# Performance work log

Measured on AMD Instinct MI355X. Metric: run time of the kernel, lower is better.

## Reference

```python
import jax, jax.numpy as jnp
import numpy as np

B, F_IN, T, N = 2, 32, 8, 20000
E = 320000
HID, F_OUT = 64, 32


def setup_inputs() -> dict:
    key = jax.random.key(0)
    ks = jax.random.split(key, 8)
    x = jax.random.normal(ks[0], (B, F_IN, T, N), dtype=jnp.float32)
    edge_index = jax.random.randint(ks[1], (2, E), 0, N, dtype=jnp.int64)
    edge_weight = jax.random.uniform(ks[2], (E,), dtype=jnp.float32)
    # GCNConv params (glorot weights, zero bias)
    s1 = float(np.sqrt(6.0 / (F_IN + HID)))
    s2 = float(np.sqrt(6.0 / (HID + F_OUT)))
    W1 = jax.random.uniform(ks[3], (F_IN, HID), minval=-s1, maxval=s1, dtype=jnp.float32)
    b1 = jnp.zeros((HID,), jnp.float32)
    W2 = jax.random.uniform(ks[4], (HID, F_OUT), minval=-s2, maxval=s2, dtype=jnp.float32)
    b2 = jnp.zeros((F_OUT,), jnp.float32)
    return {"x": x, "edge_index": edge_index, "edge_weight": edge_weight,
            "W1": W1, "b1": b1, "W2": W2, "b2": b2}


def reference(x, edge_index, edge_weight, W1, b1, W2, b2):
    Bb, Fin, Tt, Nn = x.shape
    row, col = edge_index[0], edge_index[1]
    # gcn_norm with self loops (fill value 1.0)
    loop = jnp.arange(Nn)
    row_f = jnp.concatenate([row, loop])
    col_f = jnp.concatenate([col, loop])
    ew_f = jnp.concatenate([edge_weight, jnp.ones((Nn,), x.dtype)])
    deg = jnp.zeros((Nn,), x.dtype).at[col_f].add(ew_f)
    deg_inv_sqrt = jnp.where(deg > 0, 1.0 / jnp.sqrt(jnp.where(deg > 0, deg, 1.0)), 0.0)
    norm = deg_inv_sqrt[row_f] * ew_f * deg_inv_sqrt[col_f]  # [E+N]

    # fold (batch, time) together: every time step uses the same graph
    h = x.transpose(0, 2, 3, 1).reshape(Bb * Tt, Nn, Fin)  # [BT, N, F]

    def gcn_conv(h, W, b):
        h = h @ W                                   # linear first (as in GCNConv)
        msg = h[:, row_f, :] * norm[None, :, None]  # gather + weight  [BT, E+N, C]
        agg = jnp.zeros_like(h).at[:, col_f, :].add(msg)  # scatter-add over targets
        return agg + b

    h = gcn_conv(h, W1, b1)      # dropout(p=0.1) is identity in eval mode
    h = jnp.tanh(gcn_conv(h, W2, b2))
    # back to [B, out_channels, T, N]
    return h.reshape(Bb, Tt, Nn, -1).transpose(0, 3, 1, 2)
```

## Files before the change

### kernel.cpp

```cpp
#include <hip/hip_runtime.h>
#include <hip/hip_bf16.h>
#include <hip/hip_fp16.h>

#define NB    2
#define FIN   32
#define TT    8
#define NN    20000
#define BT    16
#define CC    32
#define ROW   512
#define ELLK  64

typedef unsigned int nvec4 __attribute__((ext_vector_type(4)));

__global__ __launch_bounds__(256) void prep_kernel(const float* __restrict__ x,
                                                   __half* __restrict__ xt,
                                                   const int* __restrict__ ei,
                                                   const float* __restrict__ ew,
                                                   float* __restrict__ deg,
                                                   const float* __restrict__ W1,
                                                   const float* __restrict__ W2,
                                                   const float* __restrict__ b1,
                                                   float* __restrict__ W12T,
                                                   float* __restrict__ bb,
                                                   int N, int E, int gtr, int ge) {
    __shared__ float tile[128][33];
    int bid = blockIdx.x;
    if (bid < gtr) {
        int bt = bid & 15;
        int b = bt >> 3, t = bt & 7;
        int n0 = (bid >> 4) * 128;
        for (int i = 0; i < 16; ++i) {
            int idx = i * 256 + threadIdx.x;
            int f = idx >> 7;
            int nl = idx & 127;
            int n = n0 + nl;
            float v = (n < N) ? x[(size_t)(b * 256 + f * 8 + t) * N + n] : 0.f;
            tile[nl][f] = v;
        }
        __syncthreads();
        for (int i = 0; i < 8; ++i) {
            int idx = i * 256 + threadIdx.x;
            int nl = idx >> 4, f2 = idx & 15;
            int n = n0 + nl;
            if (n < N) {
                __half2 h = __floats2half2_rn(tile[nl][f2 * 2], tile[nl][f2 * 2 + 1]);
                *(__half2*)(xt + (size_t)n * ROW + bt * 32 + f2 * 2) = h;
            }
        }
    } else if (bid < gtr + ge) {
        int e = (bid - gtr) * 256 + threadIdx.x;
        if (e < E) {
            int c = ei[E + e];
            atomicAdd(&deg[c], ew[e]);
        }
    } else {
        for (int i = threadIdx.x; i < 1024; i += 256) {
            int f = i >> 5, c = i & 31;
            float acc = 0.f;
            for (int k = 0; k < 64; ++k) acc += W1[f * 64 + k] * W2[k * 32 + c];
            W12T[c * 32 + f] = acc;
            if (f == 0) {
                float a2 = 0.f;
                for (int k = 0; k < 64; ++k) a2 += b1[k] * W2[k * 32 + c];
                bb[c] = a2;
            }
        }
    }
}

__global__ void fill_kernel(const int* __restrict__ ei, const float* __restrict__ ew,
                            const float* __restrict__ deg,
                            int* __restrict__ fill, int2* __restrict__ ell, int E) {
    int e = blockIdx.x * 256 + threadIdx.x;
    if (e >= E) return;
    int r = ei[e], c = ei[E + e];
    float w = rsqrtf(deg[r] + 1.0f) * ew[e] * rsqrtf(deg[c] + 1.0f);
    int p = atomicAdd(&fill[c], 1);
    if (p < ELLK) ell[(size_t)c * ELLK + p] = make_int2(r, __float_as_int(w));
}

__device__ inline void unpack8n(const nvec4& u, float* f) {
    union { unsigned int v; __half2 h; } c;
    float2 a;
    c.v = u.x; a = __half22float2(c.h); f[0] = a.x; f[1] = a.y;
    c.v = u.y; a = __half22float2(c.h); f[2] = a.x; f[3] = a.y;
    c.v = u.z; a = __half22float2(c.h); f[4] = a.x; f[5] = a.y;
    c.v = u.w; a = __half22float2(c.h); f[6] = a.x; f[7] = a.y;
}

template <bool PASS1>
__global__ __launch_bounds__(256) void agg16_kernel(const __half* __restrict__ src,
                                                    __half* __restrict__ dst,
                                                    const float* __restrict__ deg,
                                                    const int* __restrict__ fillcnt,
                                                    const int2* __restrict__ ell,
                                                    float* __restrict__ rowsum,
                                                    int N) {
    int n = (blockIdx.x * 256 + threadIdx.x) >> 6;
    if (n >= N) return;
    int lane = threadIdx.x & 63;
    int cnt = fillcnt[n];
    if (cnt > ELLK) cnt = ELLK;
    float sw = 1.0f / (deg[n] + 1.0f);
    const int2* row = ell + (size_t)n * ELLK;
    float acc[8];
    {
        nvec4 u = *(const nvec4*)(src + (size_t)n * ROW + lane * 8);
        float f[8]; unpack8n(u, f);
#pragma unroll
        for (int j = 0; j < 8; ++j) acc[j] = sw * f[j];
    }
    float sumw = 0.f;
    int e = 0;
    for (; e + 8 <= cnt; e += 8) {
        long long raw[8];
#pragma unroll
        for (int j = 0; j < 8; ++j)
            raw[j] = __builtin_nontemporal_load((const long long*)(row + e + j));
        nvec4 u[8];
#pragma unroll
        for (int j = 0; j < 8; ++j) {
            unsigned int sn = (unsigned int)(raw[j] & 0xffffffffll);
            u[j] = *(const nvec4*)(src + (size_t)sn * ROW + lane * 8);
        }
#pragma unroll
        for (int j = 0; j < 8; ++j) {
            float f[8]; unpack8n(u[j], f);
            float w = __int_as_float((int)(raw[j] >> 32));
            if (PASS1) sumw += w;
#pragma unroll
            for (int q = 0; q < 8; ++q) acc[q] += w * f[q];
        }
    }
    for (; e + 2 <= cnt; e += 2) {
        long long rA = __builtin_nontemporal_load((const long long*)(row + e));
        long long rB = __builtin_nontemporal_load((const long long*)(row + e + 1));
        nvec4 uA = *(const nvec4*)(src + (size_t)(unsigned int)(rA & 0xffffffffll) * ROW + lane * 8);
        nvec4 uB = *(const nvec4*)(src + (size_t)(unsigned int)(rB & 0xffffffffll) * ROW + lane * 8);
        float fA[8], fB[8]; unpack8n(uA, fA); unpack8n(uB, fB);
        float wA = __int_as_float((int)(rA >> 32)), wB = __int_as_float((int)(rB >> 32));
        if (PASS1) sumw += wA + wB;
#pragma unroll
        for (int q = 0; q < 8; ++q) acc[q] += wA * fA[q];
#pragma unroll
        for (int q = 0; q < 8; ++q) acc[q] += wB * fB[q];
    }
    if (e < cnt) {
        long long r = __builtin_nontemporal_load((const long long*)(row + e));
        nvec4 u = *(const nvec4*)(src + (size_t)(unsigned int)(r & 0xffffffffll) * ROW + lane * 8);
        float f[8]; unpack8n(u, f);
        float w = __int_as_float((int)(r >> 32));
        if (PASS1) sumw += w;
#pragma unroll
        for (int q = 0; q < 8; ++q) acc[q] += w * f[q];
    }
    if (PASS1 && lane == 0) rowsum[n] = sw + sumw;
    union { nvec4 u; __half2 h[4]; } o;
    o.h[0] = __floats2half2_rn(acc[0], acc[1]);
    o.h[1] = __floats2half2_rn(acc[2], acc[3]);
    o.h[2] = __floats2half2_rn(acc[4], acc[5]);
    o.h[3] = __floats2half2_rn(acc[6], acc[7]);
    __builtin_nontemporal_store(o.u, (nvec4*)(dst + (size_t)n * ROW + lane * 8));
}

__global__ __launch_bounds__(256) void final_kernel(const __half* __restrict__ Z,
                                                    const float* __restrict__ W12T,
                                                    const float* __restrict__ bb,
                                                    const float* __restrict__ b2,
                                                    const float* __restrict__ rowsum,
                                                    float* __restrict__ out, int N) {
    __shared__ float zt[64][36];
    __shared__ float wT[32][36];
    __shared__ float bbs[32], b2s[32], rs[64];
    int bt = blockIdx.y;
    int b = bt >> 3, t = bt & 7;
    int n0 = blockIdx.x * 64;
    int tid = threadIdx.x;
    for (int i = tid; i < 1024; i += 256) wT[i >> 5][i & 31] = W12T[i];
    if (tid < 32) { bbs[tid] = bb[tid]; b2s[tid] = b2[tid]; }
    if (tid < 64) { int n = n0 + tid; rs[tid] = (n < N) ? rowsum[n] : 0.f; }
    for (int i = tid; i < 1024; i += 256) {
        int nl = i >> 4, f2 = i & 15;
        int n = n0 + nl;
        float2 v = make_float2(0.f, 0.f);
        if (n < N) {
            __half2 h = *(const __half2*)(Z + (size_t)n * ROW + bt * 32 + f2 * 2);
            v = __half22float2(h);
        }
        zt[nl][f2 * 2] = v.x;
        zt[nl][f2 * 2 + 1] = v.y;
    }
    __syncthreads();
    int c = tid & 31;
    int g = tid >> 5;
    float w[32];
#pragma unroll
    for (int k = 0; k < 8; ++k) {
        float4 v = *(const float4*)&wT[c][k * 4];
        w[k * 4 + 0] = v.x; w[k * 4 + 1] = v.y; w[k * 4 + 2] = v.z; w[k * 4 + 3] = v.w;
    }
    float cb2 = b2s[c], cbb = bbs[c];
    float res[8];
#pragma unroll
    for (int i = 0; i < 8; ++i) {
        int nl = g * 8 + i;
        float acc = cb2 + rs[nl] * cbb;
#pragma unroll
        for (int k = 0; k < 8; ++k) {
            float4 z4 = *(const float4*)&zt[nl][k * 4];
            acc = fmaf(z4.x, w[k * 4 + 0], acc);
            acc = fmaf(z4.y, w[k * 4 + 1], acc);
            acc = fmaf(z4.z, w[k * 4 + 2], acc);
            acc = fmaf(z4.w, w[k * 4 + 3], acc);
        }
        res[i] = tanhf(acc);
    }
    __syncthreads();
#pragma unroll
    for (int i = 0; i < 8; ++i) {
        int nl = g * 8 + i;
        zt[nl][(c + nl) & 31] = res[i];
    }
    __syncthreads();
    for (int i = tid; i < 2048; i += 256) {
        int cc = i >> 6, nl = i & 63;
        int n = n0 + nl;
        if (n < N) out[(((size_t)b * 32 + cc) * TT + t) * (size_t)NN + n] = zt[nl][(cc + nl) & 31];
    }
}

extern "C" void kernel_launch(void* const* d_in, const int* in_sizes, int n_in,
                              void* d_out, int out_size, void* d_ws, size_t ws_size,
                              hipStream_t stream) {
    const float* x  = (const float*)d_in[0];
    const int*   ei = (const int*)d_in[1];
    const float* ew = (const float*)d_in[2];
    const float* W1 = (const float*)d_in[3];
    const float* b1 = (const float*)d_in[4];
    const float* W2 = (const float*)d_in[5];
    const float* b2 = (const float*)d_in[6];
    float* out = (float*)d_out;

    const int N = NN;
    const int E = in_sizes[2];

    char* p = (char*)d_ws;
    __half* xt = (__half*)p;  p += (size_t)N * ROW * 2;
    __half* Y  = (__half*)p;  p += (size_t)N * ROW * 2;
    __half* Z  = (__half*)p;  p += (size_t)N * ROW * 2;
    int2*  ell     = (int2*)p;   p += (size_t)N * ELLK * 8;
    float* deg     = (float*)p;  p += (size_t)N * 4;
    int*   fill    = (int*)p;    p += (size_t)N * 4;
    float* rowsum  = (float*)p;  p += (size_t)N * 4;
    float* W12T    = (float*)p;  p += 1024 * 4;
    float* bb      = (float*)p;

    (void)hipMemsetAsync(deg, 0, (size_t)N * 4 * 2, stream);

    int ge  = (E + 255) / 256;
    int gtr = ((N + 127) / 128) * BT;
    prep_kernel<<<gtr + ge + 1, 256, 0, stream>>>(x, xt, ei, ew, deg,
                                                  W1, W2, b1, W12T, bb, N, E, gtr, ge);
    fill_kernel<<<ge, 256, 0, stream>>>(ei, ew, deg, fill, ell, E);

    int gagg = (N * 64 + 255) / 256;
    agg16_kernel<true ><<<gagg, 256, 0, stream>>>(xt, Y, deg, fill, ell, rowsum, N);
    agg16_kernel<false><<<gagg, 256, 0, stream>>>(Y, Z, deg, fill, ell, rowsum, N);

    dim3 gfin((N + 63) / 64, BT);
    final_kernel<<<gfin, 256, 0, stream>>>(Z, W12T, bb, b2, rowsum, out, N);
}
```

Baseline: 189.8 us.

## Fuse ELL fill into prep kernel and pack edges as 16-bit index plus fp16 weight

Removes the separate fill kernel by building the ELL adjacency inside prep_kernel, storing the raw edge weight instead of the normalized one, since degrees are not yet final at that point. Each ELL entry shrinks from 8 bytes to 4, packing a 16-bit source index with an fp16 weight. The aggregation kernels now recompute the normalization per edge from deg[src] and the destination degree. This cuts one launch and halves ELL traffic, at the cost of an extra gather of deg per edge, some rsqrt work, and fp16 weight precision. A 16-bit index cannot hold node ids above 65535; N=20000 fits, but the code would break for larger graphs.

```diff
diff --git a/kernel.cpp b/kernel.cpp
--- a/kernel.cpp
+++ b/kernel.cpp
@@ -13,11 +13,19 @@
 
 typedef unsigned int nvec4 __attribute__((ext_vector_type(4)));
 
+__device__ inline float h16tof(unsigned int hi) {
+    union { unsigned short u; __half h; } cv;
+    cv.u = (unsigned short)hi;
+    return __half2float(cv.h);
+}
+
 __global__ __launch_bounds__(256) void prep_kernel(const float* __restrict__ x,
                                                    __half* __restrict__ xt,
                                                    const int* __restrict__ ei,
                                                    const float* __restrict__ ew,
                                                    float* __restrict__ deg,
+                                                   int* __restrict__ fill,
+                                                   unsigned int* __restrict__ ell,
                                                    const float* __restrict__ W1,
                                                    const float* __restrict__ W2,
                                                    const float* __restrict__ b1,
@@ -51,8 +59,15 @@
     } else if (bid < gtr + ge) {
         int e = (bid - gtr) * 256 + threadIdx.x;
         if (e < E) {
-            int c = ei[E + e];
-            atomicAdd(&deg[c], ew[e]);
+            int r = ei[e], c = ei[E + e];
+            float wf = ew[e];
+            atomicAdd(&deg[c], wf);
+            int p = atomicAdd(&fill[c], 1);
+            if (p < ELLK) {
+                union { __half h; unsigned short u; } cv;
+                cv.h = __float2half_rn(wf);
+                ell[(size_t)c * ELLK + p] = ((unsigned int)cv.u << 16) | (unsigned int)r;
+            }
         }
     } else {
         for (int i = threadIdx.x; i < 1024; i += 256) {
@@ -69,17 +84,6 @@
     }
 }
 
-__global__ void fill_kernel(const int* __restrict__ ei, const float* __restrict__ ew,
-                            const float* __restrict__ deg,
-                            int* __restrict__ fill, int2* __restrict__ ell, int E) {
-    int e = blockIdx.x * 256 + threadIdx.x;
-    if (e >= E) return;
-    int r = ei[e], c = ei[E + e];
-    float w = rsqrtf(deg[r] + 1.0f) * ew[e] * rsqrtf(deg[c] + 1.0f);
-    int p = atomicAdd(&fill[c], 1);
-    if (p < ELLK) ell[(size_t)c * ELLK + p] = make_int2(r, __float_as_int(w));
-}
-
 __device__ inline void unpack8n(const nvec4& u, float* f) {
     union { unsigned int v; __half2 h; } c;
     float2 a;
@@ -94,7 +98,7 @@
                                                     __half* __restrict__ dst,
                                                     const float* __restrict__ deg,
                                                     const int* __restrict__ fillcnt,
-                                                    const int2* __restrict__ ell,
+                                                    const unsigned int* __restrict__ ell,
                                                     float* __restrict__ rowsum,
                                                     int N) {
     int n = (blockIdx.x * 256 + threadIdx.x) >> 6;
@@ -102,8 +106,10 @@
     int lane = threadIdx.x & 63;
     int cnt = fillcnt[n];
     if (cnt > ELLK) cnt = ELLK;
-    float sw = 1.0f / (deg[n] + 1.0f);
-    const int2* row = ell + (size_t)n * ELLK;
+    float dn = deg[n] + 1.0f;
+    float dc = rsqrtf(dn);
+    float sw = 1.0f / dn;
+    const unsigned int* row = ell + (size_t)n * ELLK;
     float acc[8];
     {
         nvec4 u = *(const nvec4*)(src + (size_t)n * ROW + lane * 8);
@@ -114,32 +120,37 @@
     float sumw = 0.f;
     int e = 0;
     for (; e + 8 <= cnt; e += 8) {
-        long long raw[8];
+        unsigned int raw[8];
 #pragma unroll
         for (int j = 0; j < 8; ++j)
-            raw[j] = __builtin_nontemporal_load((const long long*)(row + e + j));
+            raw[j] = __builtin_nontemporal_load(row + e + j);
         nvec4 u[8];
+        float dg[8];
 #pragma unroll
         for (int j = 0; j < 8; ++j) {
-            unsigned int sn = (unsigned int)(raw[j] & 0xffffffffll);
+            unsigned int sn = raw[j] & 0xffffu;
             u[j] = *(const nvec4*)(src + (size_t)sn * ROW + lane * 8);
+            dg[j] = deg[sn];
         }
 #pragma unroll
         for (int j = 0; j < 8; ++j) {
+            float w = rsqrtf(dg[j] + 1.0f) * h16tof(raw[j] >> 16) * dc;
+            if (PASS1) sumw += w;
             float f[8]; unpack8n(u[j], f);
-            float w = __int_as_float((int)(raw[j] >> 32));
-            if (PASS1) sumw += w;
 #pragma unroll
             for (int q = 0; q < 8; ++q) acc[q] += w * f[q];
         }
     }
     for (; e + 2 <= cnt; e += 2) {
-        long long rA = __builtin_nontemporal_load((const long long*)(row + e));
-        long long rB = __builtin_nontemporal_load((const long long*)(row + e + 1));
-        nvec4 uA = *(const nvec4*)(src + (size_t)(unsigned int)(rA & 0xffffffffll) * ROW + lane * 8);
-        nvec4 uB = *(const nvec4*)(src + (size_t)(unsigned int)(rB & 0xffffffffll) * ROW + lane * 8);
+        unsigned int rA = __builtin_nontemporal_load(row + e);
+        unsigned int rB = __builtin_nontemporal_load(row + e + 1);
+        unsigned int sA = rA & 0xffffu, sB = rB & 0xffffu;
+        nvec4 uA = *(const nvec4*)(src + (size_t)sA * ROW + lane * 8);
+        nvec4 uB = *(const nvec4*)(src + (size_t)sB * ROW + lane * 8);
+        float dgA = deg[sA], dgB = deg[sB];
         float fA[8], fB[8]; unpack8n(uA, fA); unpack8n(uB, fB);
-        float wA = __int_as_float((int)(rA >> 32)), wB = __int_as_float((int)(rB >> 32));
+        float wA = rsqrtf(dgA + 1.0f) * h16tof(rA >> 16) * dc;
+        float wB = rsqrtf(dgB + 1.0f) * h16tof(rB >> 16) * dc;
         if (PASS1) sumw += wA + wB;
 #pragma unroll
         for (int q = 0; q < 8; ++q) acc[q] += wA * fA[q];
@@ -147,10 +158,11 @@
         for (int q = 0; q < 8; ++q) acc[q] += wB * fB[q];
     }
     if (e < cnt) {
-        long long r = __builtin_nontemporal_load((const long long*)(row + e));
-        nvec4 u = *(const nvec4*)(src + (size_t)(unsigned int)(r & 0xffffffffll) * ROW + lane * 8);
+        unsigned int r = __builtin_nontemporal_load(row + e);
+        unsigned int sn = r & 0xffffu;
+        nvec4 u = *(const nvec4*)(src + (size_t)sn * ROW + lane * 8);
+        float w = rsqrtf(deg[sn] + 1.0f) * h16tof(r >> 16) * dc;
         float f[8]; unpack8n(u, f);
-        float w = __int_as_float((int)(r >> 32));
         if (PASS1) sumw += w;
 #pragma unroll
         for (int q = 0; q < 8; ++q) acc[q] += w * f[q];
@@ -249,7 +261,7 @@
     __half* xt = (__half*)p;  p += (size_t)N * ROW * 2;
     __half* Y  = (__half*)p;  p += (size_t)N * ROW * 2;
     __half* Z  = (__half*)p;  p += (size_t)N * ROW * 2;
-    int2*  ell     = (int2*)p;   p += (size_t)N * ELLK * 8;
+    unsigned int* ell = (unsigned int*)p; p += (size_t)N * ELLK * 4;
     float* deg     = (float*)p;  p += (size_t)N * 4;
     int*   fill    = (int*)p;    p += (size_t)N * 4;
     float* rowsum  = (float*)p;  p += (size_t)N * 4;
@@ -260,9 +272,8 @@
 
     int ge  = (E + 255) / 256;
     int gtr = ((N + 127) / 128) * BT;
-    prep_kernel<<<gtr + ge + 1, 256, 0, stream>>>(x, xt, ei, ew, deg,
+    prep_kernel<<<gtr + ge + 1, 256, 0, stream>>>(x, xt, ei, ew, deg, fill, ell,
                                                   W1, W2, b1, W12T, bb, N, E, gtr, ge);
-    fill_kernel<<<ge, 256, 0, stream>>>(ei, ew, deg, fill, ell, E);
 
     int gagg = (N * 64 + 255) / 256;
     agg16_kernel<true ><<<gagg, 256, 0, stream>>>(xt, Y, deg, fill, ell, rowsum, N);
```

Result: faster. 181.5 us (-4.4%).
